# Kernel tuning notes

Hardware: AMD Instinct MI355X
Metric: run time of the kernel (lower is better)

## Reference

```python
import jax, jax.numpy as jnp
import numpy as np
from jax import lax

IN_FEATURES = 1024
CLASSES = 512
OUT_CHANNELS = 32
N = 4096
CONV1_OUT = 32
K = 3


def setup_inputs() -> dict:
    key = jax.random.key(0)
    ks = jax.random.split(key, 7)
    s_lin = 1.0 / np.sqrt(IN_FEATURES)
    s_c1 = 1.0 / np.sqrt(1 * K)
    s_c2 = 1.0 / np.sqrt(CONV1_OUT * K)
    return {
        "x": jax.random.normal(ks[0], (N, IN_FEATURES), dtype=jnp.float32),
        "W_w": jax.random.uniform(ks[1], (CLASSES, IN_FEATURES), jnp.float32, -s_lin, s_lin),
        "W_b": jax.random.uniform(ks[2], (CLASSES,), jnp.float32, -s_lin, s_lin),
        "conv1_w": jax.random.uniform(ks[3], (CONV1_OUT, 1, K), jnp.float32, -s_c1, s_c1),
        "conv1_b": jax.random.uniform(ks[4], (CONV1_OUT,), jnp.float32, -s_c1, s_c1),
        "conv2_w": jax.random.uniform(ks[5], (OUT_CHANNELS, CONV1_OUT, K), jnp.float32, -s_c2, s_c2),
        "conv2_b": jax.random.uniform(ks[6], (OUT_CHANNELS,), jnp.float32, -s_c2, s_c2),
    }


def _conv1d(x, w, b):
    # x: [N, C_in, L], w: [C_out, C_in, K], padding=1 (same)
    y = lax.conv_general_dilated(
        x, w, window_strides=(1,), padding=((1, 1),),
        dimension_numbers=("NCH", "OIH", "NCH"))
    return y + b[None, :, None]


def reference(x, W_w, W_b, conv1_w, conv1_b, conv2_w, conv2_b):
    # SelfAttention: h = x W^T + b  -> [N, CLASSES]
    h = x @ W_w.T + W_b
    # attention = softmax(tanh(h h^T), dim=1)  -> [N, N]
    scores = jnp.tanh(h @ h.T)
    attn = jax.nn.softmax(scores, axis=1)
    a = jnp.tanh(attn @ h)                     # [N, CLASSES]
    a = jax.nn.relu(a)
    # unsqueeze(-1).permute(0,2,1): [N, CLASSES] -> [N, 1, CLASSES]
    z = a[:, None, :]
    z = jax.nn.relu(_conv1d(z, conv1_w, conv1_b))   # [N, 32, CLASSES]
    z = jax.nn.relu(_conv1d(z, conv2_w, conv2_b))   # [N, OUT_CHANNELS, CLASSES]
    return jnp.transpose(z, (0, 2, 1))              # [N, CLASSES, OUT_CHANNELS]
```

## Files before the change

### kernel.cpp

```cpp
#include <hip/hip_runtime.h>

typedef __bf16 bf16_t;
typedef __bf16 bf16x8 __attribute__((ext_vector_type(8)));
typedef __bf16 bf16x4v __attribute__((ext_vector_type(4)));
typedef float f32x4 __attribute__((ext_vector_type(4)));

__device__ __forceinline__ float tanh_fast(float x) {
  float a = fabsf(x);
  float e = __expf(-2.f * a);
  float t = (1.f - e) / (1.f + e);
  return copysignf(t, x);
}

__device__ __forceinline__ void gload16(const void* g, void* l) {
  __builtin_amdgcn_global_load_lds(
      (const __attribute__((address_space(1))) void*)g,
      (__attribute__((address_space(3))) void*)l, 16, 0, 0);
}

__global__ __launch_bounds__(256) void cast_bf16_k(const float* __restrict__ in,
                                                   bf16_t* __restrict__ out, int n4) {
  int i = blockIdx.x * 256 + threadIdx.x;
  if (i < n4) {
    float4 v = ((const float4*)in)[i];
    bf16x4v o;
    o[0] = (bf16_t)v.x; o[1] = (bf16_t)v.y; o[2] = (bf16_t)v.z; o[3] = (bf16_t)v.w;
    ((bf16x4v*)out)[i] = o;
  }
}

#define BAR() __builtin_amdgcn_s_barrier()
#define WLG() asm volatile("s_waitcnt lgkmcnt(0)" ::: "memory")
#define RDA(b, am)                                                              \
  do {                                                                          \
    _Pragma("unroll") for (int j = 0; j < 4; ++j) {                             \
      afr[j][0] = *(const bf16x8*)(pA + (b)*16384 + (am)*4096 + j*1024);        \
      afr[j][1] = *(const bf16x8*)(pA + (b)*16384 + 8192 + (am)*4096 + j*1024); \
    }                                                                           \
  } while (0)
#define RDB(b, bn)                                                              \
  do {                                                                          \
    _Pragma("unroll") for (int jj = 0; jj < 2; ++jj) {                          \
      bfr[jj][0] = *(const bf16x8*)(pB + (b)*16384 + ((bn)*2+jj)*1024);         \
      bfr[jj][1] = *(const bf16x8*)(pB + (b)*16384 + 8192 + ((bn)*2+jj)*1024);  \
    }                                                                           \
  } while (0)
#define MM16(am, bn)                                                            \
  do {                                                                          \
    __builtin_amdgcn_s_setprio(1);                                              \
    _Pragma("unroll") for (int kk = 0; kk < 2; ++kk)                            \
    _Pragma("unroll") for (int j = 0; j < 4; ++j)                               \
    _Pragma("unroll") for (int jj = 0; jj < 2; ++jj)                            \
      acc[(am)*4+j][(bn)*2+jj] = __builtin_amdgcn_mfma_f32_16x16x32_bf16(       \
          afr[j][kk], bfr[jj][kk], acc[(am)*4+j][(bn)*2+jj], 0, 0, 0);          \
    __builtin_amdgcn_s_setprio(0);                                              \
  } while (0)
#define STGA(tile, half)                                                        \
  do {                                                                          \
    const bf16_t* s_ = Ag + (size_t)(half)*128*lda + (tile)*64;                 \
    char* d_ = lds_raw + (half)*32768 + ((tile)&1)*16384 + tid*16;              \
    gload16(s_, d_); gload16(s_ + 32, d_ + 8192);                               \
  } while (0)
#define STGB(tile, half)                                                        \
  do {                                                                          \
    const bf16_t* s_ = Bg + (size_t)(half)*128*ldb + (tile)*64;                 \
    char* d_ = lds_raw + 65536 + (half)*32768 + ((tile)&1)*16384 + tid*16;      \
    gload16(s_, d_); gload16(s_ + 32, d_ + 8192);                               \
  } while (0)

template <int EPI>
__global__ __launch_bounds__(512, 2) void gemm8_k(const bf16_t* __restrict__ A,
                                                  const bf16_t* __restrict__ Bt,
                                                  bf16_t* __restrict__ out,
                                                  float* __restrict__ psum,
                                                  int lda, int ldb, int ldc,
                                                  int Klen, size_t pstride) {
  __shared__ __attribute__((aligned(16))) char lds_raw[131072];
  const int tid = threadIdx.x;
  const int wid = tid >> 6, l = tid & 63;
  const int wm = wid >> 2, wn = wid & 3;
  const int lr = l & 15, lkq = l >> 4;
  const int bx = blockIdx.x, by = blockIdx.y;
  const size_t koff = (size_t)blockIdx.z * Klen;
  const int NI = Klen >> 7;

  const int srow = tid >> 2;
  const int scol = ((tid & 3) * 8) ^ (((tid >> 5) & 1) << 4);
  const bf16_t* Ag = A + (size_t)(by * 256 + srow) * lda + koff + scol;
  const bf16_t* Bg = Bt + (size_t)(bx * 256 + srow) * ldb + koff + scol;

  const int kby = (lkq * 16) ^ (((lr >> 3) & 1) << 5);
  const char* pA = lds_raw + wm * 32768 + lr * 64 + kby;
  const char* pB = lds_raw + 65536 + (wn >> 1) * 32768 + ((wn & 1) * 64 + lr) * 64 + kby;

  bf16x8 afr[4][2], bfr[2][2];
  f32x4 acc[8][4];
#pragma unroll
  for (int m = 0; m < 8; ++m)
#pragma unroll
    for (int n = 0; n < 4; ++n) acc[m][n] = (f32x4){0.f, 0.f, 0.f, 0.f};

  STGA(0, 0); STGA(0, 1); STGB(0, 0); STGB(0, 1); STGA(1, 0);

  for (int i = 0; i < NI; ++i) {
    const int t1 = 2 * i + 1, t2 = 2 * i + 2, t3 = 2 * i + 3;
    const bool more = (i + 1 < NI);
    asm volatile("s_waitcnt vmcnt(2)" ::: "memory");
    BAR();
    RDA(0, 0); RDB(0, 0);
    STGA(t1, 1);
    WLG(); MM16(0, 0); BAR();
    RDB(0, 1); STGB(t1, 0);
    BAR(); WLG(); MM16(0, 1); BAR();
    RDA(0, 1); STGB(t1, 1);
    BAR(); WLG(); MM16(1, 1); BAR();
    RDB(0, 0);
    if (more) STGA(t2, 0);
    BAR(); WLG(); MM16(1, 0); BAR();
    if (more) { asm volatile("s_waitcnt vmcnt(2)" ::: "memory"); }
    else      { asm volatile("s_waitcnt vmcnt(0)" ::: "memory"); }
    BAR();
    RDA(1, 0); RDB(1, 0);
    if (more) STGA(t2, 1);
    WLG(); MM16(0, 0); BAR();
    RDB(1, 1);
    if (more) STGB(t2, 0);
    BAR(); WLG(); MM16(0, 1); BAR();
    RDA(1, 1);
    if (more) STGB(t2, 1);
    BAR(); WLG(); MM16(1, 1); BAR();
    RDB(1, 0);
    if (more) STGA(t3, 0);
    BAR(); WLG(); MM16(1, 0); BAR();
  }

  if constexpr (EPI == 1) {
    float* ps = psum + (size_t)(bx * 4 + wn) * 4096;
#pragma unroll
    for (int mi = 0; mi < 8; ++mi) {
#pragma unroll
      for (int v = 0; v < 4; ++v) {
        const int row = by * 256 + wm * 128 + mi * 16 + lkq * 4 + v;
        float rs = 0.f;
#pragma unroll
        for (int ni = 0; ni < 4; ++ni) {
          const int col = bx * 256 + wn * 64 + ni * 16 + lr;
          float val = __expf(tanh_fast(acc[mi][ni][v]));
          out[(size_t)row * ldc + col] = (bf16_t)val;
          rs += val;
        }
        rs += __shfl_xor(rs, 1);
        rs += __shfl_xor(rs, 2);
        rs += __shfl_xor(rs, 4);
        rs += __shfl_xor(rs, 8);
        if (lr == 0) ps[row] = rs;
      }
    }
  } else {
    bf16_t* o = out + (size_t)blockIdx.z * pstride;
#pragma unroll
    for (int mi = 0; mi < 8; ++mi)
#pragma unroll
      for (int v = 0; v < 4; ++v) {
        const int row = by * 256 + wm * 128 + mi * 16 + lkq * 4 + v;
#pragma unroll
        for (int ni = 0; ni < 4; ++ni)
          o[(size_t)row * ldc + bx * 256 + wn * 64 + ni * 16 + lr] = (bf16_t)acc[mi][ni][v];
      }
  }
}

template <int EPI>
__global__ __launch_bounds__(256) void gemm_bt_k(const bf16_t* __restrict__ A,
                                                 const bf16_t* __restrict__ Bt,
                                                 const float* __restrict__ extra,
                                                 bf16_t* __restrict__ out,
                                                 float* __restrict__ outf,
                                                 float* __restrict__ psum,
                                                 int M, int N, int Kloop, int lda, int ldb) {
  __shared__ bf16_t As[128 * 32];
  __shared__ bf16_t Bs[128 * 32];
  const int tid = threadIdx.x;
  const int w = tid >> 6;
  const int l = tid & 63;
  const int bx = blockIdx.x, by = blockIdx.y;
  const int koff = blockIdx.z * Kloop;

  const bf16_t* src = (w < 2) ? A : Bt;
  const int stride = (w < 2) ? lda : ldb;
  bf16_t* dstbase = (w < 2) ? As : Bs;
  const int tile0 = (w < 2 ? by : bx) * 128 + (w & 1) * 64;
  const int srow = l >> 2;
  const int scol = (l & 3) * 8;
  const bf16_t* gbase = src + (size_t)(tile0 + srow) * stride + scol + koff;
  bf16_t* lbase = dstbase + (w & 1) * (64 * 32);

  const int wm = w >> 1, wn = w & 1;
  const int lrow = l & 15;
  const int lk = (l >> 4) * 8;

  f32x4 zero = {0.f, 0.f, 0.f, 0.f};
  f32x4 acc[4][4];
  for (int m = 0; m < 4; ++m)
    for (int n = 0; n < 4; ++n) acc[m][n] = zero;

  for (int kt = 0; kt < Kloop; kt += 32) {
    const bf16_t* g = gbase + kt;
#pragma unroll
    for (int i = 0; i < 4; ++i) gload16(g + (size_t)i * 16 * stride, lbase + i * 512);
    __syncthreads();
    bf16x8 af[4], bfv[4];
#pragma unroll
    for (int m = 0; m < 4; ++m)
      af[m] = *(const bf16x8*)&As[(wm * 64 + m * 16 + lrow) * 32 + lk];
#pragma unroll
    for (int n = 0; n < 4; ++n)
      bfv[n] = *(const bf16x8*)&Bs[(wn * 64 + n * 16 + lrow) * 32 + lk];
#pragma unroll
    for (int m = 0; m < 4; ++m)
#pragma unroll
      for (int n = 0; n < 4; ++n)
        acc[m][n] = __builtin_amdgcn_mfma_f32_16x16x32_bf16(af[m], bfv[n], acc[m][n], 0, 0, 0);
    __syncthreads();
  }

  const int row0 = by * 128 + wm * 64;
  const int col0 = bx * 128 + wn * 64;

  if constexpr (EPI == 3) {
    float* of = outf + (size_t)blockIdx.z * M * N;
#pragma unroll
    for (int m = 0; m < 4; ++m)
#pragma unroll
      for (int v = 0; v < 4; ++v) {
        const int row = row0 + m * 16 + ((l >> 4) << 2) + v;
#pragma unroll
        for (int n = 0; n < 4; ++n)
          of[(size_t)row * N + col0 + n * 16 + lrow] = acc[m][n][v];
      }
    return;
  }

  if constexpr (EPI == 1) {
#pragma unroll
    for (int m = 0; m < 4; ++m)
#pragma unroll
      for (int v = 0; v < 4; ++v) {
        const int row = row0 + m * 16 + ((l >> 4) << 2) + v;
        float rs = 0.f;
#pragma unroll
        for (int n = 0; n < 4; ++n) {
          const int col = col0 + n * 16 + lrow;
          float val = __expf(tanh_fast(acc[m][n][v]));
          out[(size_t)row * N + col] = (bf16_t)val;
          rs += val;
        }
        if (psum) {
          rs += __shfl_xor(rs, 1);
          rs += __shfl_xor(rs, 2);
          rs += __shfl_xor(rs, 4);
          rs += __shfl_xor(rs, 8);
          if ((l & 15) == 0) psum[(size_t)(bx * 2 + wn) * M + row] = rs;
        }
      }
    return;
  }

  float bcol[4];
#pragma unroll
  for (int n = 0; n < 4; ++n)
    bcol[n] = (EPI == 0) ? extra[col0 + n * 16 + lrow] : 0.f;

#pragma unroll
  for (int m = 0; m < 4; ++m) {
#pragma unroll
    for (int v = 0; v < 4; ++v) {
      const int row = row0 + m * 16 + ((l >> 4) << 2) + v;
      float inv_dn = 1.f;
      if constexpr (EPI == 2) inv_dn = 1.f / extra[row];
#pragma unroll
      for (int n = 0; n < 4; ++n) {
        const int col = col0 + n * 16 + lrow;
        float val = acc[m][n][v];
        float o;
        if constexpr (EPI == 0) o = val + bcol[n];
        else o = fmaxf(tanh_fast(val * inv_dn), 0.f);
        out[(size_t)row * N + col] = (bf16_t)o;
      }
    }
  }
}

__global__ __launch_bounds__(256) void reduce1T_k(const float* __restrict__ p0,
                                                  const float* __restrict__ p1,
                                                  const float* __restrict__ bias,
                                                  bf16_t* __restrict__ h,
                                                  bf16_t* __restrict__ hT) {
  __shared__ bf16_t tile[64][65];
  const int d0 = blockIdx.x * 64;
  const int i0 = blockIdx.y * 64;
  const int tid = threadIdx.x;
#pragma unroll
  for (int p = 0; p < 2; ++p) {
    const int r = p * 32 + (tid >> 3);
    const int c8 = (tid & 7) * 8;
    const size_t idx = (size_t)(i0 + r) * 512 + d0 + c8;
    float4 a0 = *(const float4*)&p0[idx];
    float4 a1 = *(const float4*)&p0[idx + 4];
    float4 b0 = *(const float4*)&p1[idx];
    float4 b1 = *(const float4*)&p1[idx + 4];
    float4 w0 = *(const float4*)&bias[d0 + c8];
    float4 w1 = *(const float4*)&bias[d0 + c8 + 4];
    bf16x8 o;
    o[0] = (bf16_t)(a0.x + b0.x + w0.x);
    o[1] = (bf16_t)(a0.y + b0.y + w0.y);
    o[2] = (bf16_t)(a0.z + b0.z + w0.z);
    o[3] = (bf16_t)(a0.w + b0.w + w0.w);
    o[4] = (bf16_t)(a1.x + b1.x + w1.x);
    o[5] = (bf16_t)(a1.y + b1.y + w1.y);
    o[6] = (bf16_t)(a1.z + b1.z + w1.z);
    o[7] = (bf16_t)(a1.w + b1.w + w1.w);
    *(bf16x8*)&h[idx] = o;
#pragma unroll
    for (int k = 0; k < 8; ++k) tile[r][c8 + k] = o[k];
  }
  __syncthreads();
#pragma unroll
  for (int p = 0; p < 2; ++p) {
    const int d = p * 32 + (tid >> 3);
    const int i8 = (tid & 7) * 8;
    bf16x8 u;
#pragma unroll
    for (int k = 0; k < 8; ++k) u[k] = tile[i8 + k][d];
    *(bf16x8*)&hT[(size_t)(d0 + d) * 4096 + i0 + i8] = u;
  }
}

__global__ __launch_bounds__(256) void denred_k(const float* __restrict__ psum,
                                                float* __restrict__ den) {
  const int r = blockIdx.x * 256 + threadIdx.x;
  float s = 0.f;
#pragma unroll 8
  for (int j = 0; j < 64; ++j) s += psum[(size_t)j * 4096 + r];
  den[r] = s;
}

__global__ __launch_bounds__(256) void reduce3b_k(const bf16_t* __restrict__ pg,
                                                  const float* __restrict__ den,
                                                  bf16_t* __restrict__ t, int S) {
  const size_t i8 = (size_t)(blockIdx.x * 256 + threadIdx.x) * 8;
  float a[8] = {0.f, 0.f, 0.f, 0.f, 0.f, 0.f, 0.f, 0.f};
  for (int z = 0; z < S; ++z) {
    bf16x8 v = *(const bf16x8*)&pg[(size_t)z * (4096 * 512) + i8];
#pragma unroll
    for (int k = 0; k < 8; ++k) a[k] += (float)v[k];
  }
  const float inv = 1.f / den[i8 >> 9];
  bf16x8 o;
#pragma unroll
  for (int k = 0; k < 8; ++k) o[k] = (bf16_t)fmaxf(tanh_fast(a[k] * inv), 0.f);
  *(bf16x8*)&t[i8] = o;
}

__global__ __launch_bounds__(256) void transpose_k(const bf16_t* __restrict__ h,
                                                   bf16_t* __restrict__ hT) {
  __shared__ bf16_t tile[64][65];
  const int i0 = blockIdx.x * 64;
  const int d0 = blockIdx.y * 64;
  const int tid = threadIdx.x;
#pragma unroll
  for (int p = 0; p < 2; ++p) {
    int r = p * 32 + (tid >> 3);
    int c8 = (tid & 7) * 8;
    bf16x8 v = *(const bf16x8*)&h[(size_t)(i0 + r) * 512 + d0 + c8];
#pragma unroll
    for (int k = 0; k < 8; ++k) tile[r][c8 + k] = v[k];
  }
  __syncthreads();
#pragma unroll
  for (int p = 0; p < 2; ++p) {
    int d = p * 32 + (tid >> 3);
    int i8 = (tid & 7) * 8;
    bf16x8 u;
#pragma unroll
    for (int k = 0; k < 8; ++k) u[k] = tile[i8 + k][d];
    *(bf16x8*)&hT[(size_t)(d0 + d) * 4096 + i0 + i8] = u;
  }
}

__global__ __launch_bounds__(256) void rowsum_k(const bf16_t* __restrict__ P,
                                                float* __restrict__ den) {
  const int r = blockIdx.x;
  const int tid = threadIdx.x;
  const bf16_t* p = P + (size_t)r * 4096 + tid * 16;
  bf16x8 a = *(const bf16x8*)p;
  bf16x8 b = *(const bf16x8*)(p + 8);
  float s = 0.f;
#pragma unroll
  for (int k = 0; k < 8; ++k) s += (float)a[k] + (float)b[k];
  __shared__ float red[256];
  red[tid] = s;
  __syncthreads();
  for (int off = 128; off > 0; off >>= 1) {
    if (tid < off) red[tid] += red[tid + off];
    __syncthreads();
  }
  if (tid == 0) den[r] = red[0];
}

__global__ __launch_bounds__(256) void conv_fused_k(const bf16_t* __restrict__ t,
                                                    const float* __restrict__ w1,
                                                    const float* __restrict__ b1,
                                                    const float* __restrict__ w2,
                                                    const float* __restrict__ b2,
                                                    float* __restrict__ out) {
  __shared__ bf16_t trow[516];
  __shared__ bf16_t z1t[514 * 40];
  __shared__ bf16_t w2r[3 * 32 * 32];
  __shared__ float w1s[96], b1s[32], b2s[32];
  const int r = blockIdx.x;
  const int tid = threadIdx.x;

  if (tid < 96) w1s[tid] = w1[tid];
  if (tid < 32) { b1s[tid] = b1[tid]; b2s[tid] = b2[tid]; }
  for (int i = tid; i < 3072; i += 256) {
    int o = i / 96, rem = i % 96, c = rem / 3, kk = rem % 3;
    w2r[kk * 1024 + o * 32 + c] = (bf16_t)w2[i];
  }
  {
    const bf16_t* tp = t + (size_t)r * 512;
    trow[1 + tid] = tp[tid];
    trow[1 + 256 + tid] = tp[256 + tid];
    if (tid == 0) { trow[0] = (bf16_t)0.f; trow[513] = (bf16_t)0.f; }
    if (tid < 40) { z1t[tid] = (bf16_t)0.f; z1t[513 * 40 + tid] = (bf16_t)0.f; }
  }
  __syncthreads();

  {
    const int c = tid & 31;
    const int jb = (tid >> 5) * 64;
    const float wc0 = w1s[c * 3], wc1 = w1s[c * 3 + 1], wc2 = w1s[c * 3 + 2];
    const float bb = b1s[c];
    float tm = (float)trow[jb];
    float t0 = (float)trow[jb + 1];
    for (int j = jb; j < jb + 64; ++j) {
      float tp2 = (float)trow[j + 2];
      float v = fmaxf(bb + wc0 * tm + wc1 * t0 + wc2 * tp2, 0.f);
      z1t[(j + 1) * 40 + c] = (bf16_t)v;
      tm = t0; t0 = tp2;
    }
  }
  __syncthreads();

  const int w = tid >> 6, l = tid & 63;
  const int lrow = l & 15;
  const int lk = (l >> 4) * 8;
  bf16x8 af[3][2];
#pragma unroll
  for (int kk = 0; kk < 3; ++kk)
#pragma unroll
    for (int m = 0; m < 2; ++m)
      af[kk][m] = *(const bf16x8*)&w2r[kk * 1024 + (m * 16 + lrow) * 32 + lk];

  f32x4 zero = {0.f, 0.f, 0.f, 0.f};
  f32x4 acc[2][8];
#pragma unroll
  for (int m = 0; m < 2; ++m)
#pragma unroll
    for (int n = 0; n < 8; ++n) acc[m][n] = zero;

  const int j0 = w * 128;
#pragma unroll
  for (int kk = 0; kk < 3; ++kk) {
#pragma unroll
    for (int n = 0; n < 8; ++n) {
      bf16x8 bfv = *(const bf16x8*)&z1t[(j0 + n * 16 + lrow + kk) * 40 + lk];
      acc[0][n] = __builtin_amdgcn_mfma_f32_16x16x32_bf16(af[kk][0], bfv, acc[0][n], 0, 0, 0);
      acc[1][n] = __builtin_amdgcn_mfma_f32_16x16x32_bf16(af[kk][1], bfv, acc[1][n], 0, 0, 0);
    }
  }

#pragma unroll
  for (int m = 0; m < 2; ++m) {
    const int ob = m * 16 + ((l >> 4) << 2);
    const float bb0 = b2s[ob], bb1 = b2s[ob + 1], bb2 = b2s[ob + 2], bb3 = b2s[ob + 3];
#pragma unroll
    for (int n = 0; n < 8; ++n) {
      const int j = j0 + n * 16 + lrow;
      f32x4 res;
      res[0] = fmaxf(acc[m][n][0] + bb0, 0.f);
      res[1] = fmaxf(acc[m][n][1] + bb1, 0.f);
      res[2] = fmaxf(acc[m][n][2] + bb2, 0.f);
      res[3] = fmaxf(acc[m][n][3] + bb3, 0.f);
      *(f32x4*)&out[((size_t)r * 512 + j) * 32 + ob] = res;
    }
  }
}

extern "C" void kernel_launch(void* const* d_in, const int* in_sizes, int n_in,
                              void* d_out, int out_size, void* d_ws, size_t ws_size,
                              hipStream_t stream) {
  const float* x = (const float*)d_in[0];
  const float* Ww = (const float*)d_in[1];
  const float* Wb = (const float*)d_in[2];
  const float* c1w = (const float*)d_in[3];
  const float* c1b = (const float*)d_in[4];
  const float* c2w = (const float*)d_in[5];
  const float* c2b = (const float*)d_in[6];
  float* out = (float*)d_out;
  char* ws = (char*)d_ws;

  bf16_t* xb  = (bf16_t*)(ws + 0);
  bf16_t* Wbf = (bf16_t*)(ws + 8388608);
  bf16_t* h   = (bf16_t*)(ws + 9437184);
  bf16_t* hT  = (bf16_t*)(ws + 13631488);
  bf16_t* tb  = (bf16_t*)(ws + 17825792);
  float*  den = (float*)(ws + 22020096);

  cast_bf16_k<<<4096 * 1024 / 4 / 256, 256, 0, stream>>>(x, xb, 4096 * 1024 / 4);
  cast_bf16_k<<<512 * 1024 / 4 / 256, 256, 0, stream>>>(Ww, Wbf, 512 * 1024 / 4);

  const size_t NEED_FAST = 73416704ull;
  if (ws_size >= NEED_FAST) {
    float*  psum = (float*)(ws + 22036480);
    bf16_t* P    = (bf16_t*)(ws + 23085056);
    float*  pg1  = (float*)(ws + 23085056);
    bf16_t* pg3b = (bf16_t*)(ws + 56639488);

    gemm_bt_k<3><<<dim3(4, 32, 2), 256, 0, stream>>>(xb, Wbf, nullptr, nullptr, pg1,
                                                     nullptr, 4096, 512, 512, 1024, 1024);
    reduce1T_k<<<dim3(8, 64), 256, 0, stream>>>(pg1, pg1 + 4096 * 512, Wb, h, hT);

    gemm8_k<1><<<dim3(16, 16, 1), 512, 0, stream>>>(h, h, P, psum, 512, 512, 4096, 512, 0);
    denred_k<<<16, 256, 0, stream>>>(psum, den);

    const int S = (ws_size >= 90193920ull) ? 8 : 4;
    gemm8_k<3><<<dim3(2, 16, S), 512, 0, stream>>>(P, hT, pg3b, nullptr, 4096, 4096, 512,
                                                   4096 / S, (size_t)4096 * 512);
    reduce3b_k<<<1024, 256, 0, stream>>>(pg3b, den, tb, S);
  } else {
    bf16_t* P = (bf16_t*)(ws + 22036480);
    gemm_bt_k<0><<<dim3(4, 32), 256, 0, stream>>>(xb, Wbf, Wb, h, nullptr, nullptr,
                                                  4096, 512, 1024, 1024, 1024);
    transpose_k<<<dim3(64, 8), 256, 0, stream>>>(h, hT);
    gemm_bt_k<1><<<dim3(32, 32), 256, 0, stream>>>(h, h, nullptr, P, nullptr, nullptr,
                                                   4096, 4096, 512, 512, 512);
    rowsum_k<<<4096, 256, 0, stream>>>(P, den);
    gemm_bt_k<2><<<dim3(4, 32), 256, 0, stream>>>(P, hT, den, tb, nullptr, nullptr,
                                                  4096, 512, 4096, 4096, 4096);
  }

  conv_fused_k<<<4096, 256, 0, stream>>>(tb, c1w, c1b, c2w, c2b, out);
}
```

Baseline: 194.3 us.

## Fuse split-K reduction and denominator sum into conv kernel; merge cast launches

Combines the x/W casts and a one-time w2 reorder into a single launch. Removes the separate denominator-reduction and split-K reduce kernels by doing both inside the conv kernel per row, so the intermediate tanh/relu tensor is never written to global memory. This saves kernel launches and a round trip through memory, at the cost of strided psum reads and more work per conv block.

Result: faster. 184.8 us (-4.9%).

```diff
diff --git a/kernel.cpp b/kernel.cpp
--- a/kernel.cpp
+++ b/kernel.cpp
@@ -3,6 +3,7 @@
 typedef __bf16 bf16_t;
 typedef __bf16 bf16x8 __attribute__((ext_vector_type(8)));
 typedef __bf16 bf16x4v __attribute__((ext_vector_type(4)));
+typedef __bf16 bf16x2 __attribute__((ext_vector_type(2)));
 typedef float f32x4 __attribute__((ext_vector_type(4)));
 
 __device__ __forceinline__ float tanh_fast(float x) {
@@ -18,14 +19,31 @@
       (__attribute__((address_space(3))) void*)l, 16, 0, 0);
 }
 
-__global__ __launch_bounds__(256) void cast_bf16_k(const float* __restrict__ in,
-                                                   bf16_t* __restrict__ out, int n4) {
-  int i = blockIdx.x * 256 + threadIdx.x;
-  if (i < n4) {
-    float4 v = ((const float4*)in)[i];
+__global__ __launch_bounds__(256) void cast_all_k(const float* __restrict__ x,
+                                                  const float* __restrict__ Ww,
+                                                  const float* __restrict__ w2,
+                                                  bf16_t* __restrict__ xb,
+                                                  bf16_t* __restrict__ Wbf,
+                                                  bf16_t* __restrict__ w2rg) {
+  const int bid = blockIdx.x;
+  const int tid = threadIdx.x;
+  if (bid < 4096) {
+    const int i = bid * 256 + tid;
+    float4 v = ((const float4*)x)[i];
     bf16x4v o;
     o[0] = (bf16_t)v.x; o[1] = (bf16_t)v.y; o[2] = (bf16_t)v.z; o[3] = (bf16_t)v.w;
-    ((bf16x4v*)out)[i] = o;
+    ((bf16x4v*)xb)[i] = o;
+  } else if (bid < 4608) {
+    const int i = (bid - 4096) * 256 + tid;
+    float4 v = ((const float4*)Ww)[i];
+    bf16x4v o;
+    o[0] = (bf16_t)v.x; o[1] = (bf16_t)v.y; o[2] = (bf16_t)v.z; o[3] = (bf16_t)v.w;
+    ((bf16x4v*)Wbf)[i] = o;
+  } else {
+    for (int i = tid; i < 3072; i += 256) {
+      int o = i / 96, rem = i % 96, c = rem / 3, kk = rem % 3;
+      w2rg[kk * 1024 + o * 32 + c] = (bf16_t)w2[i];
+    }
   }
 }
 
@@ -336,32 +354,6 @@
   }
 }
 
-__global__ __launch_bounds__(256) void denred_k(const float* __restrict__ psum,
-                                                float* __restrict__ den) {
-  const int r = blockIdx.x * 256 + threadIdx.x;
-  float s = 0.f;
-#pragma unroll 8
-  for (int j = 0; j < 64; ++j) s += psum[(size_t)j * 4096 + r];
-  den[r] = s;
-}
-
-__global__ __launch_bounds__(256) void reduce3b_k(const bf16_t* __restrict__ pg,
-                                                  const float* __restrict__ den,
-                                                  bf16_t* __restrict__ t, int S) {
-  const size_t i8 = (size_t)(blockIdx.x * 256 + threadIdx.x) * 8;
-  float a[8] = {0.f, 0.f, 0.f, 0.f, 0.f, 0.f, 0.f, 0.f};
-  for (int z = 0; z < S; ++z) {
-    bf16x8 v = *(const bf16x8*)&pg[(size_t)z * (4096 * 512) + i8];
-#pragma unroll
-    for (int k = 0; k < 8; ++k) a[k] += (float)v[k];
-  }
-  const float inv = 1.f / den[i8 >> 9];
-  bf16x8 o;
-#pragma unroll
-  for (int k = 0; k < 8; ++k) o[k] = (bf16_t)fmaxf(tanh_fast(a[k] * inv), 0.f);
-  *(bf16x8*)&t[i8] = o;
-}
-
 __global__ __launch_bounds__(256) void transpose_k(const bf16_t* __restrict__ h,
                                                    bf16_t* __restrict__ hT) {
   __shared__ bf16_t tile[64][65];
@@ -408,31 +400,54 @@
   if (tid == 0) den[r] = red[0];
 }
 
-__global__ __launch_bounds__(256) void conv_fused_k(const bf16_t* __restrict__ t,
-                                                    const float* __restrict__ w1,
-                                                    const float* __restrict__ b1,
-                                                    const float* __restrict__ w2,
-                                                    const float* __restrict__ b2,
-                                                    float* __restrict__ out) {
+__global__ __launch_bounds__(256) void conv2_fused_k(const bf16_t* __restrict__ pg,
+                                                     const float* __restrict__ psum,
+                                                     const bf16_t* __restrict__ w2rg,
+                                                     const float* __restrict__ w1,
+                                                     const float* __restrict__ b1,
+                                                     const float* __restrict__ b2,
+                                                     float* __restrict__ out, int S) {
   __shared__ bf16_t trow[516];
   __shared__ bf16_t z1t[514 * 40];
-  __shared__ bf16_t w2r[3 * 32 * 32];
+  __shared__ bf16_t w2r[3072];
   __shared__ float w1s[96], b1s[32], b2s[32];
+  __shared__ float den_s;
   const int r = blockIdx.x;
   const int tid = threadIdx.x;
 
   if (tid < 96) w1s[tid] = w1[tid];
   if (tid < 32) { b1s[tid] = b1[tid]; b2s[tid] = b2[tid]; }
-  for (int i = tid; i < 3072; i += 256) {
-    int o = i / 96, rem = i % 96, c = rem / 3, kk = rem % 3;
-    w2r[kk * 1024 + o * 32 + c] = (bf16_t)w2[i];
-  }
+  ((bf16x8*)w2r)[tid] = ((const bf16x8*)w2rg)[tid];
+  if (tid < 128) ((bf16x8*)w2r)[256 + tid] = ((const bf16x8*)w2rg)[256 + tid];
+
+  if (tid < 64) {
+    float dp = psum[(size_t)tid * 4096 + r];
+    dp += __shfl_xor(dp, 32);
+    dp += __shfl_xor(dp, 16);
+    dp += __shfl_xor(dp, 8);
+    dp += __shfl_xor(dp, 4);
+    dp += __shfl_xor(dp, 2);
+    dp += __shfl_xor(dp, 1);
+    if (tid == 0) den_s = dp;
+  }
+
+  float a0 = 0.f, a1 = 0.f;
   {
-    const bf16_t* tp = t + (size_t)r * 512;
-    trow[1 + tid] = tp[tid];
-    trow[1 + 256 + tid] = tp[256 + tid];
-    if (tid == 0) { trow[0] = (bf16_t)0.f; trow[513] = (bf16_t)0.f; }
-    if (tid < 40) { z1t[tid] = (bf16_t)0.f; z1t[513 * 40 + tid] = (bf16_t)0.f; }
+    const bf16_t* pr = pg + (size_t)r * 512 + tid * 2;
+    for (int z = 0; z < S; ++z) {
+      bf16x2 v = *(const bf16x2*)(pr + (size_t)z * (4096 * 512));
+      a0 += (float)v[0];
+      a1 += (float)v[1];
+    }
+  }
+  if (tid == 0) { trow[0] = (bf16_t)0.f; trow[513] = (bf16_t)0.f; }
+  if (tid < 40) { z1t[tid] = (bf16_t)0.f; z1t[513 * 40 + tid] = (bf16_t)0.f; }
+  __syncthreads();
+
+  {
+    const float inv = 1.f / den_s;
+    trow[1 + 2 * tid] = (bf16_t)fmaxf(tanh_fast(a0 * inv), 0.f);
+    trow[2 + 2 * tid] = (bf16_t)fmaxf(tanh_fast(a1 * inv), 0.f);
   }
   __syncthreads();
 
@@ -497,6 +512,95 @@
   }
 }
 
+__global__ __launch_bounds__(256) void conv_fused_k(const bf16_t* __restrict__ t,
+                                                    const float* __restrict__ w1,
+                                                    const float* __restrict__ b1,
+                                                    const float* __restrict__ w2,
+                                                    const float* __restrict__ b2,
+                                                    float* __restrict__ out) {
+  __shared__ bf16_t trow[516];
+  __shared__ bf16_t z1t[514 * 40];
+  __shared__ bf16_t w2r[3 * 32 * 32];
+  __shared__ float w1s[96], b1s[32], b2s[32];
+  const int r = blockIdx.x;
+  const int tid = threadIdx.x;
+
+  if (tid < 96) w1s[tid] = w1[tid];
+  if (tid < 32) { b1s[tid] = b1[tid]; b2s[tid] = b2[tid]; }
+  for (int i = tid; i < 3072; i += 256) {
+    int o = i / 96, rem = i % 96, c = rem / 3, kk = rem % 3;
+    w2r[kk * 1024 + o * 32 + c] = (bf16_t)w2[i];
+  }
+  {
+    const bf16_t* tp = t + (size_t)r * 512;
+    trow[1 + tid] = tp[tid];
+    trow[1 + 256 + tid] = tp[256 + tid];
+    if (tid == 0) { trow[0] = (bf16_t)0.f; trow[513] = (bf16_t)0.f; }
+    if (tid < 40) { z1t[tid] = (bf16_t)0.f; z1t[513 * 40 + tid] = (bf16_t)0.f; }
+  }
+  __syncthreads();
+
+  {
+    const int c = tid & 31;
+    const int jb = (tid >> 5) * 64;
+    const float wc0 = w1s[c * 3], wc1 = w1s[c * 3 + 1], wc2 = w1s[c * 3 + 2];
+    const float bb = b1s[c];
+    float tm = (float)trow[jb];
+    float t0 = (float)trow[jb + 1];
+    for (int j = jb; j < jb + 64; ++j) {
+      float tp2 = (float)trow[j + 2];
+      float v = fmaxf(bb + wc0 * tm + wc1 * t0 + wc2 * tp2, 0.f);
+      z1t[(j + 1) * 40 + c] = (bf16_t)v;
+      tm = t0; t0 = tp2;
+    }
+  }
+  __syncthreads();
+
+  const int w = tid >> 6, l = tid & 63;
+  const int lrow = l & 15;
+  const int lk = (l >> 4) * 8;
+  bf16x8 af[3][2];
+#pragma unroll
+  for (int kk = 0; kk < 3; ++kk)
+#pragma unroll
+    for (int m = 0; m < 2; ++m)
+      af[kk][m] = *(const bf16x8*)&w2r[kk * 1024 + (m * 16 + lrow) * 32 + lk];
+
+  f32x4 zero = {0.f, 0.f, 0.f, 0.f};
+  f32x4 acc[2][8];
+#pragma unroll
+  for (int m = 0; m < 2; ++m)
+#pragma unroll
+    for (int n = 0; n < 8; ++n) acc[m][n] = zero;
+
+  const int j0 = w * 128;
+#pragma unroll
+  for (int kk = 0; kk < 3; ++kk) {
+#pragma unroll
+    for (int n = 0; n < 8; ++n) {
+      bf16x8 bfv = *(const bf16x8*)&z1t[(j0 + n * 16 + lrow + kk) * 40 + lk];
+      acc[0][n] = __builtin_amdgcn_mfma_f32_16x16x32_bf16(af[kk][0], bfv, acc[0][n], 0, 0, 0);
+      acc[1][n] = __builtin_amdgcn_mfma_f32_16x16x32_bf16(af[kk][1], bfv, acc[1][n], 0, 0, 0);
+    }
+  }
+
+#pragma unroll
+  for (int m = 0; m < 2; ++m) {
+    const int ob = m * 16 + ((l >> 4) << 2);
+    const float bb0 = b2s[ob], bb1 = b2s[ob + 1], bb2 = b2s[ob + 2], bb3 = b2s[ob + 3];
+#pragma unroll
+    for (int n = 0; n < 8; ++n) {
+      const int j = j0 + n * 16 + lrow;
+      f32x4 res;
+      res[0] = fmaxf(acc[m][n][0] + bb0, 0.f);
+      res[1] = fmaxf(acc[m][n][1] + bb1, 0.f);
+      res[2] = fmaxf(acc[m][n][2] + bb2, 0.f);
+      res[3] = fmaxf(acc[m][n][3] + bb3, 0.f);
+      *(f32x4*)&out[((size_t)r * 512 + j) * 32 + ob] = res;
+    }
+  }
+}
+
 extern "C" void kernel_launch(void* const* d_in, const int* in_sizes, int n_in,
                               void* d_out, int out_size, void* d_ws, size_t ws_size,
                               hipStream_t stream) {
@@ -515,10 +619,10 @@
   bf16_t* h   = (bf16_t*)(ws + 9437184);
   bf16_t* hT  = (bf16_t*)(ws + 13631488);
   bf16_t* tb  = (bf16_t*)(ws + 17825792);
+  bf16_t* w2rg = (bf16_t*)(ws + 17825792);
   float*  den = (float*)(ws + 22020096);
 
-  cast_bf16_k<<<4096 * 1024 / 4 / 256, 256, 0, stream>>>(x, xb, 4096 * 1024 / 4);
-  cast_bf16_k<<<512 * 1024 / 4 / 256, 256, 0, stream>>>(Ww, Wbf, 512 * 1024 / 4);
+  cast_all_k<<<4609, 256, 0, stream>>>(x, Ww, c2w, xb, Wbf, w2rg);
 
   const size_t NEED_FAST = 73416704ull;
   if (ws_size >= NEED_FAST) {
@@ -532,12 +636,12 @@
     reduce1T_k<<<dim3(8, 64), 256, 0, stream>>>(pg1, pg1 + 4096 * 512, Wb, h, hT);
 
     gemm8_k<1><<<dim3(16, 16, 1), 512, 0, stream>>>(h, h, P, psum, 512, 512, 4096, 512, 0);
-    denred_k<<<16, 256, 0, stream>>>(psum, den);
 
     const int S = (ws_size >= 90193920ull) ? 8 : 4;
     gemm8_k<3><<<dim3(2, 16, S), 512, 0, stream>>>(P, hT, pg3b, nullptr, 4096, 4096, 512,
                                                    4096 / S, (size_t)4096 * 512);
-    reduce3b_k<<<1024, 256, 0, stream>>>(pg3b, den, tb, S);
+
+    conv2_fused_k<<<4096, 256, 0, stream>>>(pg3b, psum, w2rg, c1w, c1b, c2b, out, S);
   } else {
     bf16_t* P = (bf16_t*)(ws + 22036480);
     gemm_bt_k<0><<<dim3(4, 32), 256, 0, stream>>>(xb, Wbf, Wb, h, nullptr, nullptr,
@@ -548,7 +652,6 @@
     rowsum_k<<<4096, 256, 0, stream>>>(P, den);
     gemm_bt_k<2><<<dim3(4, 32), 256, 0, stream>>>(P, hT, den, tb, nullptr, nullptr,
                                                   4096, 512, 4096, 4096, 4096);
-  }
-
-  conv_fused_k<<<4096, 256, 0, stream>>>(tb, c1w, c1b, c2w, c2b, out);
-}
+    conv_fused_k<<<4096, 256, 0, stream>>>(tb, c1w, c1b, c2w, c2b, out);
+  }
+}
```
